# Kernel optimization log

Hardware: AMD Instinct MI355X
Metric: run time of the kernel (lower is better)

## Reference

```python
import jax, jax.numpy as jnp
import numpy as np

B, S, E, H = 8, 2048, 512, 8
D = E // H  # head_dim = 64


def setup_inputs() -> dict:
    key0 = jax.random.key(0)
    ks = jax.random.split(key0, 12)
    scale = 1.0 / np.sqrt(E)
    return {
        "value": jax.random.normal(ks[0], (B, S, E), jnp.float32),
        "key": jax.random.normal(ks[1], (B, S, E), jnp.float32),
        "query": jax.random.normal(ks[2], (B, S, E), jnp.float32),
        "mask": jax.random.randint(ks[3], (B, 1, 1, S), 0, 2, jnp.int32),
        "wq": jax.random.normal(ks[4], (E, E), jnp.float32) * scale,
        "bq": jnp.zeros((E,), jnp.float32),
        "wk": jax.random.normal(ks[5], (E, E), jnp.float32) * scale,
        "bk": jnp.zeros((E,), jnp.float32),
        "wv": jax.random.normal(ks[6], (E, E), jnp.float32) * scale,
        "bv": jnp.zeros((E,), jnp.float32),
        "wo": jax.random.normal(ks[7], (E, E), jnp.float32) * scale,
        "bo": jnp.zeros((E,), jnp.float32),
    }


def reference(value, key, query, mask, wq, bq, wk, bk, wv, bv, wo, bo):
    b, s, e = query.shape
    # projections
    q = (query @ wq + bq).reshape(b, s, H, D)  # (B,S,H,D)
    k = (key @ wk + bk).reshape(b, s, H, D)
    v = (value @ wv + bv).reshape(b, s, H, D)
    # scaled dot-product logits: (B,H,Sq,Sk)
    logits = jnp.einsum("bqhd,bkhd->bhqk", q, k) / jnp.sqrt(jnp.asarray(D, q.dtype))
    logits = logits + mask.astype(logits.dtype) * -1e9  # mask==1 -> blocked
    attn = jax.nn.softmax(logits, axis=-1)
    out = jnp.einsum("bhqk,bkhd->bqhd", attn, v).reshape(b, s, e)
    return out @ wo + bo
```

## Files before the change

### kernel.cpp

```cpp
#include <hip/hip_runtime.h>

#define Bz 8
#define Sz 2048
#define Ez 512
#define Hz 8
#define Dz 64

typedef _Float16 f16;
typedef __attribute__((ext_vector_type(2))) _Float16 f16x2;
typedef __attribute__((ext_vector_type(8))) _Float16 f16x8;
typedef __attribute__((ext_vector_type(4))) float f32x4;

#define LOG2E 1.44269504f

__device__ __forceinline__ void async16(const void* g, void* l) {
    __builtin_amdgcn_global_load_lds(
        (const __attribute__((address_space(1))) unsigned int*)g,
        (__attribute__((address_space(3))) unsigned int*)l, 16, 0, 0);
}

__device__ __forceinline__ f16x2 pkrtz(float a, float b) {
    return __builtin_bit_cast(f16x2, __builtin_amdgcn_cvt_pkrtz(a, b));
}

__device__ __forceinline__ int swz(int row) {
    return (row & 7) ^ ((2 * ((row >> 3) & 3)) & 7);
}

__global__ __launch_bounds__(256)
void cast_kernel(const float* __restrict__ q, const float* __restrict__ k,
                 const float* __restrict__ v, const int* __restrict__ mask,
                 f16* __restrict__ qa, f16* __restrict__ ka, f16* __restrict__ va,
                 int* __restrict__ idx, int* __restrict__ slen, f16* __restrict__ vt)
{
    const int blk = blockIdx.x;
    const int tid = threadIdx.x;
    if (blk >= 2048) {
        const int b = blk - 2048;
        if (b >= Bz) return;
        __shared__ int sc2[2][256];
        __shared__ int ssl;
        const int* mp = mask + (size_t)b * Sz;
        int m[8], c = 0;
        #pragma unroll
        for (int j = 0; j < 8; ++j) { m[j] = mp[tid*8 + j]; c += (m[j] == 0); }
        sc2[0][tid] = c;
        __syncthreads();
        int src = 0;
        #pragma unroll
        for (int s = 1; s < 256; s <<= 1) {
            int vv = sc2[src][tid] + ((tid >= s) ? sc2[src][tid - s] : 0);
            sc2[src ^ 1][tid] = vv;
            src ^= 1;
            __syncthreads();
        }
        int incl = sc2[src][tid];
        int base = incl - c;
        if (tid == 255) { slen[b] = incl; ssl = incl; }
        int kk = base;
        #pragma unroll
        for (int j = 0; j < 8; ++j)
            if (m[j] == 0) idx[(size_t)b * Sz + (kk++)] = tid*8 + j;
        __syncthreads();
        const int sl2 = ssl;
        const int pad = (sl2 + 63) & ~63;
        if (pad > sl2) {
            for (int pr = tid; pr < Hz * Dz; pr += 256) {
                f16* dst = vt + ((size_t)b * Hz * Dz + pr) * Sz;
                for (int j = sl2; j < pad; ++j) dst[j] = (f16)0.f;
            }
        }
        return;
    }
    const unsigned CPT = 1u << 20;
    for (unsigned c = blk * 256 + tid; c < 3 * CPT; c += 2048 * 256) {
        const unsigned z = c >> 20;
        const size_t off = (size_t)(c & (CPT - 1)) * 8;
        const float* s = (z == 0) ? q : (z == 1) ? k : v;
        f16* dst = (z == 0) ? qa : (z == 1) ? ka : va;
        float4 x0 = *(const float4*)&s[off];
        float4 x1 = *(const float4*)&s[off + 4];
        f16 h[8];
        f16x2 p0 = pkrtz(x0.x, x0.y), p1 = pkrtz(x0.z, x0.w);
        f16x2 p2 = pkrtz(x1.x, x1.y), p3 = pkrtz(x1.z, x1.w);
        h[0] = p0[0]; h[1] = p0[1]; h[2] = p1[0]; h[3] = p1[1];
        h[4] = p2[0]; h[5] = p2[1]; h[6] = p3[0]; h[7] = p3[1];
        *(uint4*)&dst[off] = *(uint4*)h;
    }
}

__global__ __launch_bounds__(256)
void prep_w(const float* __restrict__ W0, const float* __restrict__ W1,
            const float* __restrict__ W2, const float* __restrict__ W3,
            f16* __restrict__ T0, f16* __restrict__ T1,
            f16* __restrict__ T2, f16* __restrict__ T3)
{
    __shared__ float S[64][68];
    const float* W = (blockIdx.z==0)?W0:(blockIdx.z==1)?W1:(blockIdx.z==2)?W2:W3;
    f16*         T = (blockIdx.z==0)?T0:(blockIdx.z==1)?T1:(blockIdx.z==2)?T2:T3;
    const float sc = (blockIdx.z == 0) ? 0.125f * LOG2E : 1.0f;
    const int k0 = blockIdx.x * 64, n0 = blockIdx.y * 64;
    const int tid = threadIdx.x;
    {
        int kr = tid >> 4, nc = (tid & 15) * 4;
        #pragma unroll
        for (int i = 0; i < 4; ++i) {
            float4 w4 = *(const float4*)&W[(size_t)(k0 + kr + i*16) * Ez + n0 + nc];
            S[kr + i*16][nc+0] = w4.x; S[kr + i*16][nc+1] = w4.y;
            S[kr + i*16][nc+2] = w4.z; S[kr + i*16][nc+3] = w4.w;
        }
    }
    __syncthreads();
    {
        int n = tid >> 2, kq = tid & 3;
        f16 h[16];
        #pragma unroll
        for (int j = 0; j < 16; ++j) h[j] = (f16)(S[kq*16 + j][n] * sc);
        f16* dst = &T[(size_t)(n0 + n) * Ez + k0 + kq*16];
        *(uint4*)&dst[0] = *(uint4*)&h[0];
        *(uint4*)&dst[8] = *(uint4*)&h[8];
    }
}

__global__ __launch_bounds__(256, 4)
void proj_gemm(const f16* __restrict__ qa, const f16* __restrict__ ka,
               const f16* __restrict__ va,
               const f16* __restrict__ wtq, const f16* __restrict__ wtk,
               const f16* __restrict__ wtv,
               const float* __restrict__ bqp, const float* __restrict__ bkp,
               const float* __restrict__ bvp, const int* __restrict__ idx,
               const int* __restrict__ slen,
               f16* __restrict__ qp, f16* __restrict__ kp, f16* __restrict__ vt)
{
    __shared__ __align__(16) char lds[32768];
    const int z = blockIdx.z;
    const int m0 = blockIdx.x * 128, n0 = blockIdx.y * 128;
    const int bb = m0 >> 11;
    const int m0c = m0 & (Sz - 1);

    int sl = Sz;
    if (z != 0) {
        sl = slen[bb];
        if (m0c >= sl) return;
    }

    const f16* A  = (z==0)?qa:(z==1)?ka:va;
    const f16* Wt = (z==0)?wtq:(z==1)?wtk:wtv;
    const float* bias = (z==0)?bqp:(z==1)?bkp:bvp;
    const float bscale = (z==0) ? 0.125f*LOG2E : 1.0f;

    const int tid  = threadIdx.x;
    const int lane = tid & 63, w = tid >> 6;
    const int col  = lane & 15, quad = lane >> 4;
    const int wm = w & 1, wn = w >> 1;
    const int srow = lane >> 2, schunk = lane & 3;

    size_t rb[2];
    int clv[2];
    #pragma unroll
    for (int i = 0; i < 2; ++i) {
        const int row = w*32 + i*16 + srow;
        clv[i] = schunk ^ ((row >> 1) & 3);
        const int j = m0c + row;
        int srcrow;
        if (z == 0) {
            srcrow = j;
        } else {
            const int jc = (j < sl) ? j : sl - 1;
            srcrow = idx[(size_t)bb * Sz + jc];
        }
        rb[i] = ((size_t)bb * Sz + srcrow) * Ez;
    }

    f32x4 acc[4][4];
    #pragma unroll
    for (int i = 0; i < 4; ++i)
        #pragma unroll
        for (int j = 0; j < 4; ++j) acc[i][j] = (f32x4){0.f,0.f,0.f,0.f};

    auto issue = [&](int t, int buf) {
        f16* As = (f16*)(lds + buf * 16384);
        f16* Ws = As + 4096;
        #pragma unroll
        for (int i = 0; i < 2; ++i) {
            const int row = w*32 + i*16 + srow;
            async16(&A[rb[i] + t*32 + clv[i]*8],                    &As[row*32 + schunk*8]);
            async16(&Wt[(size_t)(n0 + row) * Ez + t*32 + clv[i]*8], &Ws[row*32 + schunk*8]);
        }
    };

    issue(0, 0);
    const int xrc = (col >> 1) & 3;

    for (int t = 0; t < 16; ++t) {
        const int cur = t & 1;
        __syncthreads();
        if (t < 15) issue(t + 1, cur ^ 1);
        f16* As = (f16*)(lds + cur * 16384);
        f16* Ws = As + 4096;
        f16x8 af[4];
        #pragma unroll
        for (int mi = 0; mi < 4; ++mi)
            af[mi] = *(const f16x8*)&As[(wm*64 + mi*16 + col)*32 + ((quad ^ xrc)*8)];
        #pragma unroll
        for (int ni = 0; ni < 4; ++ni) {
            f16x8 wf = *(const f16x8*)&Ws[(wn*64 + ni*16 + col)*32 + ((quad ^ xrc)*8)];
            #pragma unroll
            for (int mi = 0; mi < 4; ++mi)
                acc[mi][ni] = __builtin_amdgcn_mfma_f32_16x16x32_f16(af[mi], wf, acc[mi][ni], 0,0,0);
        }
    }

    const int rw = tid >> 1, half = tid & 1;

    f16* Tr  = (f16*)lds;
    f16* Tr2 = (f16*)lds;
    #pragma unroll
    for (int p = 0; p < 2; ++p) {
        __syncthreads();
        if (wn == p) {
            #pragma unroll
            for (int ni = 0; ni < 4; ++ni) {
                float bv = bias[n0 + p*64 + ni*16 + col] * bscale;
                #pragma unroll
                for (int mi = 0; mi < 4; ++mi)
                    #pragma unroll
                    for (int rr = 0; rr < 4; ++rr) {
                        const int ml = wm*64 + mi*16 + quad*4 + rr;
                        const float val = acc[mi][ni][rr] + bv;
                        if (z != 2) Tr[ml*72 + ni*16 + col] = (f16)val;
                        else        Tr2[(ni*16 + col)*136 + ml] = (f16)val;
                    }
            }
        }
        __syncthreads();
        const int hh = (n0 >> 6) + p;
        if (z != 2) {
            const int rank = m0c + rw;
            if (z == 0 || rank < sl) {
                f16* C16 = (z == 0) ? qp : kp;
                f16* dst = &C16[(((size_t)bb*Hz + hh)*Sz + rank)*Dz + half*32];
                const f16* srcp = &Tr[rw*72 + half*32];
                #pragma unroll
                for (int j = 0; j < 4; ++j)
                    *(uint4*)&dst[j*8] = *(const uint4*)&srcp[j*8];
            }
        } else {
            const int d = tid >> 2, mq = tid & 3;
            const int base = m0c + mq*32;
            if (base < sl) {
                f16* dstb = vt + (((size_t)bb*Hz + hh)*Dz + d)*Sz + base;
                const f16* srcr = &Tr2[d*136 + mq*32];
                int lim = sl - base; if (lim > 32) lim = 32;
                if (lim == 32) {
                    #pragma unroll
                    for (int g = 0; g < 4; ++g)
                        *(uint4*)&dstb[g*8] = *(const uint4*)&srcr[g*8];
                } else {
                    const int full = lim >> 3;
                    for (int g = 0; g < full; ++g)
                        *(uint4*)&dstb[g*8] = *(const uint4*)&srcr[g*8];
                    for (int e = full*8; e < lim; ++e) dstb[e] = srcr[e];
                }
            }
        }
    }
}

__global__ __launch_bounds__(256, 4)
void out_gemm(const f16* __restrict__ A, const f16* __restrict__ Wt,
              const float* __restrict__ bias, float* __restrict__ Cf)
{
    __shared__ __align__(16) char lds[32768];
    const int tid  = threadIdx.x;
    const int lane = tid & 63, w = tid >> 6;
    const int col  = lane & 15, quad = lane >> 4;
    const int wm = w & 1, wn = w >> 1;
    const int m0 = blockIdx.x * 128, n0 = blockIdx.y * 128;
    const int srow = lane >> 2, schunk = lane & 3;

    f32x4 acc[4][4];
    #pragma unroll
    for (int i = 0; i < 4; ++i)
        #pragma unroll
        for (int j = 0; j < 4; ++j) acc[i][j] = (f32x4){0.f,0.f,0.f,0.f};

    auto issue = [&](int t, int buf) {
        f16* As = (f16*)(lds + buf * 16384);
        f16* Ws = As + 4096;
        #pragma unroll
        for (int i = 0; i < 2; ++i) {
            int row = w*32 + i*16 + srow;
            int cl = schunk ^ ((row >> 1) & 3);
            async16(&A[(size_t)(m0 + row) * Ez + t*32 + cl*8],  &As[row*32 + schunk*8]);
            async16(&Wt[(size_t)(n0 + row) * Ez + t*32 + cl*8], &Ws[row*32 + schunk*8]);
        }
    };

    issue(0, 0);
    const int xrc = (col >> 1) & 3;

    for (int t = 0; t < 16; ++t) {
        const int cur = t & 1;
        __syncthreads();
        if (t < 15) issue(t + 1, cur ^ 1);
        f16* As = (f16*)(lds + cur * 16384);
        f16* Ws = As + 4096;
        f16x8 af[4];
        #pragma unroll
        for (int mi = 0; mi < 4; ++mi)
            af[mi] = *(const f16x8*)&As[(wm*64 + mi*16 + col)*32 + ((quad ^ xrc)*8)];
        #pragma unroll
        for (int ni = 0; ni < 4; ++ni) {
            f16x8 wf = *(const f16x8*)&Ws[(wn*64 + ni*16 + col)*32 + ((quad ^ xrc)*8)];
            #pragma unroll
            for (int mi = 0; mi < 4; ++mi)
                acc[mi][ni] = __builtin_amdgcn_mfma_f32_16x16x32_f16(af[mi], wf, acc[mi][ni], 0,0,0);
        }
    }

    #pragma unroll
    for (int ni = 0; ni < 4; ++ni) {
        int n = n0 + wn*64 + ni*16 + col;
        float bv = bias[n];
        #pragma unroll
        for (int mi = 0; mi < 4; ++mi)
            #pragma unroll
            for (int rr = 0; rr < 4; ++rr) {
                int m = m0 + wm*64 + mi*16 + quad*4 + rr;
                Cf[(size_t)m * Ez + n] = acc[mi][ni][rr] + bv;
            }
    }
}

__global__ __launch_bounds__(256, 4)
void attn_f16(const f16* __restrict__ Q, const f16* __restrict__ K,
              const f16* __restrict__ VT, const int* __restrict__ slen,
              f16* __restrict__ O)
{
    __shared__ __align__(16) f16 KS[2][64*64];
    __shared__ __align__(16) f16 VS[2][64*64];

    const int tid  = threadIdx.x;
    const int lane = tid & 63, w = tid >> 6;
    const int col  = lane & 15, quad = lane >> 4;

    const int blk = blockIdx.x;
    const int xcd = blk & 7, slot = blk >> 3;
    const int bh = xcd + 8 * (slot >> 4);
    const int qb = slot & 15;
    const int b = bh >> 3, h = bh & 7;

    const int sl = slen[b];
    int nt = (sl + 63) >> 6;
    if (nt < 1) nt = 1;

    const int q0 = qb * 128 + w * 32;

    f16x8 qf[2][2];
    #pragma unroll
    for (int qt = 0; qt < 2; ++qt)
        #pragma unroll
        for (int ks = 0; ks < 2; ++ks)
            qf[qt][ks] = *(const f16x8*)&Q[((size_t)bh*Sz + q0 + qt*16 + col)*Dz + ks*32 + quad*8];

    const f16* Kp = K + (size_t)bh * Sz * Dz;
    const f16* Vp = VT + (size_t)bh * Dz * Sz;

    const int srow = lane >> 3, sch = lane & 7;
    const int row0 = w*16 + srow, row1 = row0 + 8;
    const int cl0 = sch ^ swz(row0), cl1 = sch ^ swz(row1);

    int keyrow[4], gk[4];
    #pragma unroll
    for (int kc = 0; kc < 4; ++kc) {
        keyrow[kc] = 32*(kc>>1) + 8*(col>>2) + 4*(kc&1) + (col&3);
        gk[kc] = swz(keyrow[kc]);
    }

    f32x4 oacc[2][4];
    #pragma unroll
    for (int qt = 0; qt < 2; ++qt)
        #pragma unroll
        for (int dc = 0; dc < 4; ++dc) oacc[qt][dc] = (f32x4){0.f,0.f,0.f,0.f};
    const f32x4 zero4 = (f32x4){0.f, 0.f, 0.f, 0.f};
    f32x4 lacc[2] = {(f32x4){0.f,0.f,0.f,0.f}, (f32x4){0.f,0.f,0.f,0.f}};
    f16x8 one8;
    #pragma unroll
    for (int i = 0; i < 8; ++i) one8[i] = (f16)1.0f;

    auto issue = [&](int t, int buf) {
        async16(&Kp[(size_t)(t*64 + row0)*Dz + cl0*8], &KS[buf][row0*64 + sch*8]);
        async16(&Vp[(size_t)row0*Sz + t*64 + cl0*8],   &VS[buf][row0*64 + sch*8]);
        async16(&Kp[(size_t)(t*64 + row1)*Dz + cl1*8], &KS[buf][row1*64 + sch*8]);
        async16(&Vp[(size_t)row1*Sz + t*64 + cl1*8],   &VS[buf][row1*64 + sch*8]);
    };

    issue(0, 0);

    for (int t = 0; t < nt; ++t) {
        const int cur = t & 1;
        __syncthreads();
        if (t + 1 < nt) issue(t + 1, cur ^ 1);

        f32x4 sc[2][4];
        __builtin_amdgcn_s_setprio(1);
        #pragma unroll
        for (int kc = 0; kc < 4; ++kc) {
            f16x8 kf0 = *(const f16x8*)&KS[cur][keyrow[kc]*64 + ((quad ^ gk[kc])*8)];
            f16x8 kf1 = *(const f16x8*)&KS[cur][keyrow[kc]*64 + (((4 + quad) ^ gk[kc])*8)];
            sc[0][kc] = __builtin_amdgcn_mfma_f32_16x16x32_f16(kf0, qf[0][0], zero4, 0,0,0);
            sc[1][kc] = __builtin_amdgcn_mfma_f32_16x16x32_f16(kf0, qf[1][0], zero4, 0,0,0);
            sc[0][kc] = __builtin_amdgcn_mfma_f32_16x16x32_f16(kf1, qf[0][1], sc[0][kc], 0,0,0);
            sc[1][kc] = __builtin_amdgcn_mfma_f32_16x16x32_f16(kf1, qf[1][1], sc[1][kc], 0,0,0);
        }
        __builtin_amdgcn_s_setprio(0);

        const bool last = (t == nt - 1);
        union { f16x2 h2[4]; f16x8 h8; } ph[2][2];
        #pragma unroll
        for (int qt = 0; qt < 2; ++qt) {
            #pragma unroll
            for (int kg = 0; kg < 2; ++kg) {
                float e0 = __builtin_amdgcn_exp2f(sc[qt][2*kg][0]);
                float e1 = __builtin_amdgcn_exp2f(sc[qt][2*kg][1]);
                float e2 = __builtin_amdgcn_exp2f(sc[qt][2*kg][2]);
                float e3 = __builtin_amdgcn_exp2f(sc[qt][2*kg][3]);
                float e4 = __builtin_amdgcn_exp2f(sc[qt][2*kg+1][0]);
                float e5 = __builtin_amdgcn_exp2f(sc[qt][2*kg+1][1]);
                float e6 = __builtin_amdgcn_exp2f(sc[qt][2*kg+1][2]);
                float e7 = __builtin_amdgcn_exp2f(sc[qt][2*kg+1][3]);
                if (last) {
                    int rem = sl - t*64 - 32*kg - 8*quad;
                    e0 = (rem > 0) ? e0 : 0.f; e1 = (rem > 1) ? e1 : 0.f;
                    e2 = (rem > 2) ? e2 : 0.f; e3 = (rem > 3) ? e3 : 0.f;
                    e4 = (rem > 4) ? e4 : 0.f; e5 = (rem > 5) ? e5 : 0.f;
                    e6 = (rem > 6) ? e6 : 0.f; e7 = (rem > 7) ? e7 : 0.f;
                }
                ph[qt][kg].h2[0] = pkrtz(e0, e1);
                ph[qt][kg].h2[1] = pkrtz(e2, e3);
                ph[qt][kg].h2[2] = pkrtz(e4, e5);
                ph[qt][kg].h2[3] = pkrtz(e6, e7);
            }
        }

        __builtin_amdgcn_s_setprio(1);
        lacc[0] = __builtin_amdgcn_mfma_f32_16x16x32_f16(one8, ph[0][0].h8, lacc[0], 0,0,0);
        lacc[1] = __builtin_amdgcn_mfma_f32_16x16x32_f16(one8, ph[1][0].h8, lacc[1], 0,0,0);
        lacc[0] = __builtin_amdgcn_mfma_f32_16x16x32_f16(one8, ph[0][1].h8, lacc[0], 0,0,0);
        lacc[1] = __builtin_amdgcn_mfma_f32_16x16x32_f16(one8, ph[1][1].h8, lacc[1], 0,0,0);
        #pragma unroll
        for (int dc = 0; dc < 4; ++dc) {
            const int d = dc*16 + col;
            const int gd = swz(d);
            #pragma unroll
            for (int kg = 0; kg < 2; ++kg) {
                f16x8 vf = *(const f16x8*)&VS[cur][d*64 + (((kg*4 + quad) ^ gd)*8)];
                oacc[0][dc] = __builtin_amdgcn_mfma_f32_16x16x32_f16(vf, ph[0][kg].h8, oacc[0][dc], 0,0,0);
                oacc[1][dc] = __builtin_amdgcn_mfma_f32_16x16x32_f16(vf, ph[1][kg].h8, oacc[1][dc], 0,0,0);
            }
        }
        __builtin_amdgcn_s_setprio(0);
    }

    float inv[2];
    inv[0] = 1.0f / lacc[0][0];
    inv[1] = 1.0f / lacc[1][0];
    #pragma unroll
    for (int qt = 0; qt < 2; ++qt) {
        const int q = q0 + qt*16 + col;
        f16* op = &O[((size_t)b*Sz + q)*Ez + h*Dz];
        #pragma unroll
        for (int dc = 0; dc < 4; ++dc) {
            f16 ov[4] = {(f16)(oacc[qt][dc][0]*inv[qt]), (f16)(oacc[qt][dc][1]*inv[qt]),
                         (f16)(oacc[qt][dc][2]*inv[qt]), (f16)(oacc[qt][dc][3]*inv[qt])};
            *(uint2*)&op[dc*16 + quad*4] = *(uint2*)ov;
        }
    }
}

extern "C" void kernel_launch(void* const* d_in, const int* in_sizes, int n_in,
                              void* d_out, int out_size, void* d_ws, size_t ws_size,
                              hipStream_t stream)
{
    const float* value = (const float*)d_in[0];
    const float* key   = (const float*)d_in[1];
    const float* query = (const float*)d_in[2];
    const int*   mask  = (const int*)d_in[3];
    const float* wq = (const float*)d_in[4];
    const float* bq = (const float*)d_in[5];
    const float* wk = (const float*)d_in[6];
    const float* bk = (const float*)d_in[7];
    const float* wv = (const float*)d_in[8];
    const float* bv = (const float*)d_in[9];
    const float* wo = (const float*)d_in[10];
    const float* bo = (const float*)d_in[11];
    float* out = (float*)d_out;

    const size_t nW   = (size_t)Ez * Ez;
    const size_t nAct = (size_t)Bz * Sz * Ez;
    f16* wtq = (f16*)d_ws;
    f16* wtk = wtq + nW;
    f16* wtv = wtk + nW;
    f16* wto = wtv + nW;
    f16* qa  = wto + nW;
    f16* ka  = qa + nAct;
    f16* va  = ka + nAct;
    f16* qp  = va + nAct;
    f16* kp  = qp + nAct;
    f16* vt  = kp + nAct;
    f16* o16 = vt + nAct;
    int* idxp = (int*)(o16 + nAct);
    int* slenp = idxp + Bz * Sz;

    cast_kernel<<<2056, 256, 0, stream>>>(query, key, value, mask,
                                          qa, ka, va, idxp, slenp, vt);
    prep_w<<<dim3(8, 8, 4), 256, 0, stream>>>(wq, wk, wv, wo, wtq, wtk, wtv, wto);

    proj_gemm<<<dim3(128, 4, 3), 256, 0, stream>>>(qa, ka, va, wtq, wtk, wtv,
                                                   bq, bk, bv, idxp, slenp,
                                                   qp, kp, vt);

    attn_f16<<<1024, 256, 0, stream>>>(qp, kp, vt, slenp, o16);

    out_gemm<<<dim3(128, 4), 256, 0, stream>>>(o16, wto, bo, out);
}
```

Before: 279.2 us.

## Compact masked key/value rows during the cast instead of in the projection GEMM

The mask scan and index build now run first, in a kernel merged with the weight transpose. The cast kernel then converts only the unmasked key/value rows into a compacted fp16 buffer, using one wave per row. Because of this, proj_gemm loads contiguous rows and no longer needs an index gather. The aim is to skip reading and writing masked K/V rows in the cast pass and to simplify GEMM address generation; the cost is that the cast now has to wait for the mask scan, plus a larger, partly idle grid.

New measurement: 275.7 us. Within noise of the previous version (-1.3%).

```diff
diff --git a/kernel.cpp b/kernel.cpp
--- a/kernel.cpp
+++ b/kernel.cpp
@@ -28,98 +28,119 @@
 }
 
 __global__ __launch_bounds__(256)
-void cast_kernel(const float* __restrict__ q, const float* __restrict__ k,
-                 const float* __restrict__ v, const int* __restrict__ mask,
-                 f16* __restrict__ qa, f16* __restrict__ ka, f16* __restrict__ va,
-                 int* __restrict__ idx, int* __restrict__ slen, f16* __restrict__ vt)
+void prep_kernel(const float* __restrict__ W0, const float* __restrict__ W1,
+                 const float* __restrict__ W2, const float* __restrict__ W3,
+                 f16* __restrict__ T0, f16* __restrict__ T1,
+                 f16* __restrict__ T2, f16* __restrict__ T3,
+                 const int* __restrict__ mask, int* __restrict__ idx,
+                 int* __restrict__ slen, f16* __restrict__ vt)
 {
     const int blk = blockIdx.x;
     const int tid = threadIdx.x;
-    if (blk >= 2048) {
-        const int b = blk - 2048;
-        if (b >= Bz) return;
-        __shared__ int sc2[2][256];
-        __shared__ int ssl;
-        const int* mp = mask + (size_t)b * Sz;
-        int m[8], c = 0;
-        #pragma unroll
-        for (int j = 0; j < 8; ++j) { m[j] = mp[tid*8 + j]; c += (m[j] == 0); }
-        sc2[0][tid] = c;
-        __syncthreads();
-        int src = 0;
-        #pragma unroll
-        for (int s = 1; s < 256; s <<= 1) {
-            int vv = sc2[src][tid] + ((tid >= s) ? sc2[src][tid - s] : 0);
-            sc2[src ^ 1][tid] = vv;
-            src ^= 1;
-            __syncthreads();
-        }
-        int incl = sc2[src][tid];
-        int base = incl - c;
-        if (tid == 255) { slen[b] = incl; ssl = incl; }
-        int kk = base;
-        #pragma unroll
-        for (int j = 0; j < 8; ++j)
-            if (m[j] == 0) idx[(size_t)b * Sz + (kk++)] = tid*8 + j;
-        __syncthreads();
-        const int sl2 = ssl;
-        const int pad = (sl2 + 63) & ~63;
-        if (pad > sl2) {
-            for (int pr = tid; pr < Hz * Dz; pr += 256) {
-                f16* dst = vt + ((size_t)b * Hz * Dz + pr) * Sz;
-                for (int j = sl2; j < pad; ++j) dst[j] = (f16)0.f;
-            }
+    if (blk < 256) {
+        __shared__ float S[64][68];
+        const int z = blk >> 6, rest = blk & 63;
+        const float* W = (z==0)?W0:(z==1)?W1:(z==2)?W2:W3;
+        f16*         T = (z==0)?T0:(z==1)?T1:(z==2)?T2:T3;
+        const float sc = (z == 0) ? 0.125f * LOG2E : 1.0f;
+        const int k0 = (rest & 7) * 64, n0 = (rest >> 3) * 64;
+        {
+            int kr = tid >> 4, nc = (tid & 15) * 4;
+            #pragma unroll
+            for (int i = 0; i < 4; ++i) {
+                float4 w4 = *(const float4*)&W[(size_t)(k0 + kr + i*16) * Ez + n0 + nc];
+                S[kr + i*16][nc+0] = w4.x; S[kr + i*16][nc+1] = w4.y;
+                S[kr + i*16][nc+2] = w4.z; S[kr + i*16][nc+3] = w4.w;
+            }
+        }
+        __syncthreads();
+        {
+            int n = tid >> 2, kq = tid & 3;
+            f16 h[16];
+            #pragma unroll
+            for (int j = 0; j < 16; ++j) h[j] = (f16)(S[kq*16 + j][n] * sc);
+            f16* dst = &T[(size_t)(n0 + n) * Ez + k0 + kq*16];
+            *(uint4*)&dst[0] = *(uint4*)&h[0];
+            *(uint4*)&dst[8] = *(uint4*)&h[8];
         }
         return;
     }
-    const unsigned CPT = 1u << 20;
-    for (unsigned c = blk * 256 + tid; c < 3 * CPT; c += 2048 * 256) {
-        const unsigned z = c >> 20;
-        const size_t off = (size_t)(c & (CPT - 1)) * 8;
-        const float* s = (z == 0) ? q : (z == 1) ? k : v;
-        f16* dst = (z == 0) ? qa : (z == 1) ? ka : va;
-        float4 x0 = *(const float4*)&s[off];
-        float4 x1 = *(const float4*)&s[off + 4];
+    const int b = blk - 256;
+    if (b >= Bz) return;
+    __shared__ int sc2[2][256];
+    __shared__ int ssl;
+    const int* mp = mask + (size_t)b * Sz;
+    int m[8], c = 0;
+    #pragma unroll
+    for (int j = 0; j < 8; ++j) { m[j] = mp[tid*8 + j]; c += (m[j] == 0); }
+    sc2[0][tid] = c;
+    __syncthreads();
+    int src = 0;
+    #pragma unroll
+    for (int s = 1; s < 256; s <<= 1) {
+        int vv = sc2[src][tid] + ((tid >= s) ? sc2[src][tid - s] : 0);
+        sc2[src ^ 1][tid] = vv;
+        src ^= 1;
+        __syncthreads();
+    }
+    int incl = sc2[src][tid];
+    int base = incl - c;
+    if (tid == 255) { slen[b] = incl; ssl = incl; }
+    int kk = base;
+    #pragma unroll
+    for (int j = 0; j < 8; ++j)
+        if (m[j] == 0) idx[(size_t)b * Sz + (kk++)] = tid*8 + j;
+    __syncthreads();
+    const int sl2 = ssl;
+    const int pad = (sl2 + 63) & ~63;
+    if (pad > sl2) {
+        for (int pr = tid; pr < Hz * Dz; pr += 256) {
+            f16* dst = vt + ((size_t)b * Hz * Dz + pr) * Sz;
+            for (int j = sl2; j < pad; ++j) dst[j] = (f16)0.f;
+        }
+    }
+}
+
+__global__ __launch_bounds__(256)
+void cast_kernel(const float* __restrict__ q, const float* __restrict__ key,
+                 const float* __restrict__ value, const int* __restrict__ idx,
+                 const int* __restrict__ slen,
+                 f16* __restrict__ qa, f16* __restrict__ ka, f16* __restrict__ va)
+{
+    const int blk = blockIdx.x;
+    const int tid = threadIdx.x;
+    if (blk < 4096) {
+        const size_t off = ((size_t)blk * 256 + tid) * 8;
+        float4 x0 = *(const float4*)&q[off];
+        float4 x1 = *(const float4*)&q[off + 4];
         f16 h[8];
         f16x2 p0 = pkrtz(x0.x, x0.y), p1 = pkrtz(x0.z, x0.w);
         f16x2 p2 = pkrtz(x1.x, x1.y), p3 = pkrtz(x1.z, x1.w);
         h[0] = p0[0]; h[1] = p0[1]; h[2] = p1[0]; h[3] = p1[1];
         h[4] = p2[0]; h[5] = p2[1]; h[6] = p3[0]; h[7] = p3[1];
-        *(uint4*)&dst[off] = *(uint4*)h;
-    }
-}
-
-__global__ __launch_bounds__(256)
-void prep_w(const float* __restrict__ W0, const float* __restrict__ W1,
-            const float* __restrict__ W2, const float* __restrict__ W3,
-            f16* __restrict__ T0, f16* __restrict__ T1,
-            f16* __restrict__ T2, f16* __restrict__ T3)
-{
-    __shared__ float S[64][68];
-    const float* W = (blockIdx.z==0)?W0:(blockIdx.z==1)?W1:(blockIdx.z==2)?W2:W3;
-    f16*         T = (blockIdx.z==0)?T0:(blockIdx.z==1)?T1:(blockIdx.z==2)?T2:T3;
-    const float sc = (blockIdx.z == 0) ? 0.125f * LOG2E : 1.0f;
-    const int k0 = blockIdx.x * 64, n0 = blockIdx.y * 64;
-    const int tid = threadIdx.x;
-    {
-        int kr = tid >> 4, nc = (tid & 15) * 4;
-        #pragma unroll
-        for (int i = 0; i < 4; ++i) {
-            float4 w4 = *(const float4*)&W[(size_t)(k0 + kr + i*16) * Ez + n0 + nc];
-            S[kr + i*16][nc+0] = w4.x; S[kr + i*16][nc+1] = w4.y;
-            S[kr + i*16][nc+2] = w4.z; S[kr + i*16][nc+3] = w4.w;
-        }
-    }
-    __syncthreads();
-    {
-        int n = tid >> 2, kq = tid & 3;
-        f16 h[16];
-        #pragma unroll
-        for (int j = 0; j < 16; ++j) h[j] = (f16)(S[kq*16 + j][n] * sc);
-        f16* dst = &T[(size_t)(n0 + n) * Ez + k0 + kq*16];
-        *(uint4*)&dst[0] = *(uint4*)&h[0];
-        *(uint4*)&dst[8] = *(uint4*)&h[8];
-    }
+        *(uint4*)&qa[off] = *(uint4*)h;
+        return;
+    }
+    const int r = blk - 4096;
+    const int zt = r >> 12;
+    const int rem = r & 4095;
+    const int b = rem >> 9, grp = rem & 511;
+    const int sl = slen[b];
+    if (grp * 4 >= sl) return;
+    const int w = tid >> 6, lane = tid & 63;
+    const int j = grp * 4 + w;
+    if (j >= sl) return;
+    const int s = idx[(size_t)b * Sz + j];
+    const float* srcp = ((zt == 0) ? key : value) + ((size_t)b * Sz + s) * Ez + lane * 8;
+    f16* dst = ((zt == 0) ? ka : va) + ((size_t)b * Sz + j) * Ez + lane * 8;
+    float4 x0 = *(const float4*)&srcp[0];
+    float4 x1 = *(const float4*)&srcp[4];
+    f16 h[8];
+    f16x2 p0 = pkrtz(x0.x, x0.y), p1 = pkrtz(x0.z, x0.w);
+    f16x2 p2 = pkrtz(x1.x, x1.y), p3 = pkrtz(x1.z, x1.w);
+    h[0] = p0[0]; h[1] = p0[1]; h[2] = p1[0]; h[3] = p1[1];
+    h[4] = p2[0]; h[5] = p2[1]; h[6] = p3[0]; h[7] = p3[1];
+    *(uint4*)&dst[lane * 0] = *(uint4*)h;
 }
 
 __global__ __launch_bounds__(256, 4)
@@ -128,8 +149,7 @@
                const f16* __restrict__ wtq, const f16* __restrict__ wtk,
                const f16* __restrict__ wtv,
                const float* __restrict__ bqp, const float* __restrict__ bkp,
-               const float* __restrict__ bvp, const int* __restrict__ idx,
-               const int* __restrict__ slen,
+               const float* __restrict__ bvp, const int* __restrict__ slen,
                f16* __restrict__ qp, f16* __restrict__ kp, f16* __restrict__ vt)
 {
     __shared__ __align__(16) char lds[32768];
@@ -155,23 +175,6 @@
     const int wm = w & 1, wn = w >> 1;
     const int srow = lane >> 2, schunk = lane & 3;
 
-    size_t rb[2];
-    int clv[2];
-    #pragma unroll
-    for (int i = 0; i < 2; ++i) {
-        const int row = w*32 + i*16 + srow;
-        clv[i] = schunk ^ ((row >> 1) & 3);
-        const int j = m0c + row;
-        int srcrow;
-        if (z == 0) {
-            srcrow = j;
-        } else {
-            const int jc = (j < sl) ? j : sl - 1;
-            srcrow = idx[(size_t)bb * Sz + jc];
-        }
-        rb[i] = ((size_t)bb * Sz + srcrow) * Ez;
-    }
-
     f32x4 acc[4][4];
     #pragma unroll
     for (int i = 0; i < 4; ++i)
@@ -184,8 +187,9 @@
         #pragma unroll
         for (int i = 0; i < 2; ++i) {
             const int row = w*32 + i*16 + srow;
-            async16(&A[rb[i] + t*32 + clv[i]*8],                    &As[row*32 + schunk*8]);
-            async16(&Wt[(size_t)(n0 + row) * Ez + t*32 + clv[i]*8], &Ws[row*32 + schunk*8]);
+            const int cl = schunk ^ ((row >> 1) & 3);
+            async16(&A[(size_t)(m0 + row) * Ez + t*32 + cl*8],  &As[row*32 + schunk*8]);
+            async16(&Wt[(size_t)(n0 + row) * Ez + t*32 + cl*8], &Ws[row*32 + schunk*8]);
         }
     };
 
@@ -513,12 +517,14 @@
     int* idxp = (int*)(o16 + nAct);
     int* slenp = idxp + Bz * Sz;
 
-    cast_kernel<<<2056, 256, 0, stream>>>(query, key, value, mask,
-                                          qa, ka, va, idxp, slenp, vt);
-    prep_w<<<dim3(8, 8, 4), 256, 0, stream>>>(wq, wk, wv, wo, wtq, wtk, wtv, wto);
+    prep_kernel<<<264, 256, 0, stream>>>(wq, wk, wv, wo, wtq, wtk, wtv, wto,
+                                         mask, idxp, slenp, vt);
+
+    cast_kernel<<<12288, 256, 0, stream>>>(query, key, value, idxp, slenp,
+                                           qa, ka, va);
 
     proj_gemm<<<dim3(128, 4, 3), 256, 0, stream>>>(qa, ka, va, wtq, wtk, wtv,
-                                                   bq, bk, bv, idxp, slenp,
+                                                   bq, bk, bv, slenp,
                                                    qp, kp, vt);
 
     attn_f16<<<1024, 256, 0, stream>>>(qp, kp, vt, slenp, o16);
```
